# Kernel optimization log

Hardware: AMD Instinct MI355X
Metric: run time of the kernel (lower is better)

The kernel has to match this reference:

```python
import jax, jax.numpy as jnp
import numpy as np

LN_EPS = 1e-5
N_HEADS = 8

def _layernorm(x, g, b):
    mu = jnp.mean(x, axis=-1, keepdims=True)
    var = jnp.var(x, axis=-1, keepdims=True)
    return (x - mu) * jax.lax.rsqrt(var + LN_EPS) * g + b

def _posenc(seqlen, d_model, dtype):
    den = jnp.exp(-jnp.arange(0, d_model, 2, dtype=dtype) * (np.log(10000.0) / d_model))
    pos = jnp.arange(seqlen, dtype=dtype)[:, None]  # [S,1]
    pe = jnp.zeros((seqlen, d_model), dtype=dtype)
    pe = pe.at[:, 0::2].set(jnp.sin(pos * den))
    pe = pe.at[:, 1::2].set(jnp.cos(pos * den)[:, : d_model // 2])
    return pe  # [S,d]

def setup_inputs() -> dict:
    key = jax.random.key(0)
    ks = jax.random.split(key, 12)
    B, S, V, D, F, L, DL = 64, 256, 16, 512, 2048, 6, 256
    s = 0.05
    return {
        "src_pad": jax.random.normal(ks[0], (B, S, V), jnp.float32),
        "emb_w": jax.random.normal(ks[1], (D, V), jnp.float32) * s,
        "emb_b": jnp.zeros((D,), jnp.float32),
        "qkv_w": jax.random.normal(ks[2], (L, 3 * D, D), jnp.float32) * s,
        "qkv_b": jnp.zeros((L, 3 * D), jnp.float32),
        "out_w": jax.random.normal(ks[3], (L, D, D), jnp.float32) * s,
        "out_b": jnp.zeros((L, D), jnp.float32),
        "ff1_w": jax.random.normal(ks[4], (L, F, D), jnp.float32) * s,
        "ff1_b": jnp.zeros((L, F), jnp.float32),
        "ff2_w": jax.random.normal(ks[5], (L, D, F), jnp.float32) * s,
        "ff2_b": jnp.zeros((L, D), jnp.float32),
        "ln1_g": jnp.ones((L, D), jnp.float32),
        "ln1_b": jnp.zeros((L, D), jnp.float32),
        "ln2_g": jnp.ones((L, D), jnp.float32),
        "ln2_b": jnp.zeros((L, D), jnp.float32),
        "lat_w": jax.random.normal(ks[6], (DL, S * D), jnp.float32) * 0.005,
        "lat_b": jnp.zeros((DL,), jnp.float32),
        "head_w": jax.random.normal(ks[7], (1, DL), jnp.float32) * s,
        "head_b": jnp.zeros((1,), jnp.float32),
    }

def reference(src_pad, emb_w, emb_b, qkv_w, qkv_b, out_w, out_b,
              ff1_w, ff1_b, ff2_w, ff2_b, ln1_g, ln1_b, ln2_g, ln2_b,
              lat_w, lat_b, head_w, head_b):
    B, S, V = src_pad.shape
    D = emb_w.shape[0]
    L = qkv_w.shape[0]
    H = N_HEADS
    dh = D // H
    # batched replacement of the per-token Python-loop embedding
    x = jnp.einsum('bsv,dv->bsd', src_pad, emb_w) + emb_b
    x = x + _posenc(S, D, x.dtype)  # dropout is identity at eval
    scale = 1.0 / np.sqrt(dh)
    for l in range(L):  # post-norm PyTorch TransformerEncoderLayer, relu FFN
        qkv = jnp.einsum('bsd,ed->bse', x, qkv_w[l]) + qkv_b[l]  # [B,S,3D]
        q, k, v = jnp.split(qkv, 3, axis=-1)
        q = q.reshape(B, S, H, dh).transpose(0, 2, 1, 3)
        k = k.reshape(B, S, H, dh).transpose(0, 2, 1, 3)
        v = v.reshape(B, S, H, dh).transpose(0, 2, 1, 3)
        attn = jax.nn.softmax(jnp.einsum('bhqd,bhkd->bhqk', q, k) * scale, axis=-1)
        o = jnp.einsum('bhqk,bhkd->bhqd', attn, v).transpose(0, 2, 1, 3).reshape(B, S, D)
        o = jnp.einsum('bsd,ed->bse', o, out_w[l]) + out_b[l]
        x = _layernorm(x + o, ln1_g[l], ln1_b[l])
        h = jax.nn.relu(jnp.einsum('bsd,fd->bsf', x, ff1_w[l]) + ff1_b[l])
        h = jnp.einsum('bsf,df->bsd', h, ff2_w[l]) + ff2_b[l]
        x = _layernorm(x + h, ln2_g[l], ln2_b[l])
    mem = x.reshape(B, S * D) @ lat_w.T + lat_b  # [B, d_latent]
    pred = jax.nn.sigmoid(mem @ head_w.T + head_b)  # [B,1]
    return pred
```

## Files before the change

### kernel.cpp

```cpp
#include <hip/hip_runtime.h>
#include <hip/hip_bf16.h>
#include <cstdint>

#define DEV static __device__ __forceinline__

typedef __attribute__((ext_vector_type(8))) short bf16x8;
typedef __attribute__((ext_vector_type(4))) float f32x4;

DEV unsigned short f2bf(float f) {
  union { float f; unsigned u; } c; c.f = f;
  unsigned u = c.u;
  return (unsigned short)((u + 0x7fffu + ((u >> 16) & 1u)) >> 16);
}
DEV float bf2f(unsigned short h) {
  union { unsigned u; float f; } c; c.u = ((unsigned)h) << 16; return c.f;
}
DEV float bflo(unsigned u) { union { unsigned u; float f; } c; c.u = u << 16; return c.f; }
DEV float bfhi(unsigned u) { union { unsigned u; float f; } c; c.u = u & 0xffff0000u; return c.f; }
DEV unsigned pack_bf16(float a, float b) {
  union { float f; unsigned u; } ca, cb; ca.f = a; cb.f = b;
  return __builtin_amdgcn_perm(cb.u + 0x8000u, ca.u + 0x8000u, 0x07060302u);
}

#define ASYNC_COPY16(gsrc, ldst)                                                      \
  __builtin_amdgcn_global_load_lds(                                                   \
      (const __attribute__((address_space(1))) void*)(unsigned long long)(gsrc),      \
      (__attribute__((address_space(3))) void*)(unsigned int)(unsigned long long)(ldst), \
      16, 0, 0)

__global__ void cvt4_kernel(const float* __restrict__ s, unsigned short* __restrict__ d) {
  size_t i = ((size_t)blockIdx.x * 256 + threadIdx.x) * 4;
  float4 v = *(const float4*)(s + i);
  d[i + 0] = f2bf(v.x);
  d[i + 1] = f2bf(v.y);
  d[i + 2] = f2bf(v.z);
  d[i + 3] = f2bf(v.w);
}

__global__ void embed_kernel(const float* __restrict__ src,
                             const float* __restrict__ emb_w,
                             const float* __restrict__ emb_b,
                             unsigned short* __restrict__ xb) {
  const int bs = blockIdx.x;
  const int d = threadIdx.x;
  const int s = bs & 255;
  __shared__ float sv[16];
  if (d < 16) sv[d] = src[(size_t)bs * 16 + d];
  __syncthreads();
  const float* wr = emb_w + (size_t)d * 16;
  float acc = emb_b[d];
#pragma unroll
  for (int v = 0; v < 16; v++) acc += sv[v] * wr[v];
  const float den = __expf(-(float)(d & ~1) * (9.2103403719761836f / 512.f));
  const float arg = (float)s * den;
  acc += (d & 1) ? __cosf(arg) : __sinf(arg);
  xb[(size_t)bs * 512 + d] = f2bf(acc);
}

template <int BN, int MINW, int RELU, int OUT_BF16, int ADD_RES>
__global__ __launch_bounds__(256, MINW) void gemm_nt(
    const unsigned short* __restrict__ A,
    const unsigned short* __restrict__ B,
    const float* __restrict__ bias,
    const unsigned short* __restrict__ res,
    float* __restrict__ Cf,
    unsigned short* __restrict__ Cb,
    int M, int N, int K) {
  constexpr int MT = (BN == 128) ? 4 : 2;
  constexpr int NT = 4;
  __shared__ unsigned short As[128 * 64];
  __shared__ unsigned short Bs[BN * 64];
  const int tid = threadIdx.x;
  const int lane = tid & 63;
  const int w = tid >> 6;
  const int m0 = blockIdx.x * 128;
  const int n0 = blockIdx.y * BN;

  const int srow = lane >> 3;
  const int scol = (((lane & 7) ^ srow)) * 8;
  const unsigned short* gA0 = A + (size_t)(m0 + w * 32 + srow) * K + scol;
  unsigned short* lA0 = As + (w * 32) * 64;
  constexpr int BROWS = BN / 4 / 8;
  const unsigned short* gB0 = B + (size_t)(n0 + w * (BN / 4) + srow) * K + scol;
  unsigned short* lB0 = Bs + (w * (BN / 4)) * 64;

  const int wm = (BN == 128) ? (w >> 1) * 64 : w * 32;
  const int wn = (BN == 128) ? (w & 1) * 64 : 0;
  const int r16 = lane & 15;
  const int quad = lane >> 4;
  const int rsw = r16 & 7;

  f32x4 acc[MT][NT] = {};

  for (int k0 = 0; k0 < K; k0 += 64) {
#pragma unroll
    for (int i = 0; i < 4; i++)
      ASYNC_COPY16(gA0 + (size_t)(i * 8) * K + k0, lA0 + i * 512);
#pragma unroll
    for (int i = 0; i < BROWS; i++)
      ASYNC_COPY16(gB0 + (size_t)(i * 8) * K + k0, lB0 + i * 512);
    __syncthreads();
#pragma unroll
    for (int kh = 0; kh < 2; kh++) {
      const int ko = ((kh * 4 + quad) ^ rsw) * 8;
      bf16x8 xa[MT], wb[NT];
#pragma unroll
      for (int i = 0; i < MT; i++)
        xa[i] = *(const bf16x8*)(As + (wm + i * 16 + r16) * 64 + ko);
#pragma unroll
      for (int j = 0; j < NT; j++)
        wb[j] = *(const bf16x8*)(Bs + (wn + j * 16 + r16) * 64 + ko);
#pragma unroll
      for (int i = 0; i < MT; i++)
#pragma unroll
        for (int j = 0; j < NT; j++)
          acc[i][j] = __builtin_amdgcn_mfma_f32_16x16x32_bf16(wb[j], xa[i], acc[i][j], 0, 0, 0);
    }
    __syncthreads();
  }

  const int mb = m0 + wm + r16;
  const int nb = n0 + wn + quad * 4;
#pragma unroll
  for (int j = 0; j < NT; j++) {
    const int n = nb + j * 16;
    const float4 bv = *(const float4*)(bias + n);
#pragma unroll
    for (int i = 0; i < MT; i++) {
      const size_t off = (size_t)(mb + i * 16) * N + n;
      float4 v;
      v.x = acc[i][j][0] + bv.x;
      v.y = acc[i][j][1] + bv.y;
      v.z = acc[i][j][2] + bv.z;
      v.w = acc[i][j][3] + bv.w;
      if (ADD_RES) {
        const uint2 ru = *(const uint2*)(res + off);
        v.x += bflo(ru.x); v.y += bfhi(ru.x);
        v.z += bflo(ru.y); v.w += bfhi(ru.y);
      }
      if (RELU) {
        v.x = fmaxf(v.x, 0.f); v.y = fmaxf(v.y, 0.f);
        v.z = fmaxf(v.z, 0.f); v.w = fmaxf(v.w, 0.f);
      }
      if (OUT_BF16) {
        uint2 u;
        u.x = pack_bf16(v.x, v.y);
        u.y = pack_bf16(v.z, v.w);
        *(uint2*)(Cb + off) = u;
      } else {
        *(float4*)(Cf + off) = v;
      }
    }
  }
}

__global__ __launch_bounds__(256, 2) void attn_fused(
    const unsigned short* __restrict__ qkv,
    unsigned short* __restrict__ O) {
  __shared__ unsigned short Vt[64 * 264];
  __shared__ unsigned short Pl[32 * 264];
  __shared__ float redM[4][32];
  __shared__ float redS[4][32];
  const int tid = threadIdx.x;
  const int lane = tid & 63;
  const int w = tid >> 6;
  const int r16 = lane & 15;
  const int quad = lane >> 4;
  const int h = blockIdx.x & 7;
  const int b = blockIdx.x >> 3;

  {
    const int kp = w * 32 + (lane & 31);
    const int dhalf = lane >> 5;
    const unsigned short* vbase =
        qkv + (size_t)(b * 256 + 2 * kp) * 1536 + 1024 + h * 64;
    unsigned* dst = (unsigned*)Vt;
#pragma unroll
    for (int t = 0; t < 4; t++) {
      const int dc = dhalf + 2 * t;
      const uint4 a = *(const uint4*)(vbase + dc * 8);
      const uint4 bb = *(const uint4*)(vbase + 1536 + dc * 8);
      const unsigned* ap = (const unsigned*)&a;
      const unsigned* bp = (const unsigned*)&bb;
#pragma unroll
      for (int i = 0; i < 4; i++) {
        const unsigned lo = ap[i], hi = bp[i];
        dst[(dc * 8 + 2 * i) * 132 + kp] = (lo & 0xffffu) | (hi << 16);
        dst[(dc * 8 + 2 * i + 1) * 132 + kp] = (lo >> 16) | (hi & 0xffff0000u);
      }
    }
  }
  __syncthreads();

  const unsigned short* krow =
      qkv + (size_t)(b * 256 + r16) * 1536 + 512 + h * 64 + quad * 8;
  const unsigned short* qrow =
      qkv + (size_t)(b * 256 + r16) * 1536 + h * 64 + quad * 8;

  for (int qt = 0; qt < 8; qt++) {
    const int q0 = qt * 32;
    f32x4 acc[4][2] = {};
    bf16x8 bQ0[2], bQ1[2];
#pragma unroll
    for (int nt = 0; nt < 2; nt++) {
      const unsigned short* qp = qrow + (size_t)(q0 + nt * 16) * 1536;
      bQ0[nt] = *(const bf16x8*)(qp);
      bQ1[nt] = *(const bf16x8*)(qp + 32);
    }
#pragma unroll
    for (int mt = 0; mt < 4; mt++) {
      const unsigned short* kp = krow + (size_t)(w * 64 + mt * 16) * 1536;
      const bf16x8 aK0 = *(const bf16x8*)(kp);
      const bf16x8 aK1 = *(const bf16x8*)(kp + 32);
#pragma unroll
      for (int nt = 0; nt < 2; nt++) {
        acc[mt][nt] = __builtin_amdgcn_mfma_f32_16x16x32_bf16(aK0, bQ0[nt], acc[mt][nt], 0, 0, 0);
        acc[mt][nt] = __builtin_amdgcn_mfma_f32_16x16x32_bf16(aK1, bQ1[nt], acc[mt][nt], 0, 0, 0);
      }
    }
#pragma unroll
    for (int nt = 0; nt < 2; nt++) {
      float m = acc[0][nt][0];
#pragma unroll
      for (int mt = 0; mt < 4; mt++)
#pragma unroll
        for (int r = 0; r < 4; r++) m = fmaxf(m, acc[mt][nt][r]);
      m = fmaxf(m, __shfl_xor(m, 16));
      m = fmaxf(m, __shfl_xor(m, 32));
      if (quad == 0) redM[w][nt * 16 + r16] = m;
    }
    __syncthreads();
    float mg[2], sw[2];
#pragma unroll
    for (int nt = 0; nt < 2; nt++) {
      const int q = nt * 16 + r16;
      mg[nt] = fmaxf(fmaxf(redM[0][q], redM[1][q]), fmaxf(redM[2][q], redM[3][q]));
      sw[nt] = 0.f;
    }
#pragma unroll
    for (int mt = 0; mt < 4; mt++)
#pragma unroll
      for (int nt = 0; nt < 2; nt++)
#pragma unroll
        for (int r = 0; r < 4; r++) {
          acc[mt][nt][r] = __expf((acc[mt][nt][r] - mg[nt]) * 0.125f);
          sw[nt] += acc[mt][nt][r];
        }
#pragma unroll
    for (int nt = 0; nt < 2; nt++) {
      sw[nt] += __shfl_xor(sw[nt], 16);
      sw[nt] += __shfl_xor(sw[nt], 32);
      if (quad == 0) redS[w][nt * 16 + r16] = sw[nt];
    }
    __syncthreads();
    float inv[2];
#pragma unroll
    for (int nt = 0; nt < 2; nt++) {
      const int q = nt * 16 + r16;
      inv[nt] = 1.f / (redS[0][q] + redS[1][q] + redS[2][q] + redS[3][q]);
    }
#pragma unroll
    for (int nt = 0; nt < 2; nt++) {
      unsigned short* prow = Pl + (nt * 16 + r16) * 264 + w * 64 + quad * 4;
#pragma unroll
      for (int mt = 0; mt < 4; mt++) {
        uint2 u;
        u.x = pack_bf16(acc[mt][nt][0] * inv[nt], acc[mt][nt][1] * inv[nt]);
        u.y = pack_bf16(acc[mt][nt][2] * inv[nt], acc[mt][nt][3] * inv[nt]);
        *(uint2*)(prow + mt * 16) = u;
      }
    }
    __syncthreads();
    f32x4 o[2] = {};
#pragma unroll
    for (int s = 0; s < 8; s++) {
      const bf16x8 aV = *(const bf16x8*)(Vt + (w * 16 + r16) * 264 + s * 32 + quad * 8);
#pragma unroll
      for (int nt = 0; nt < 2; nt++) {
        const bf16x8 bP = *(const bf16x8*)(Pl + (nt * 16 + r16) * 264 + s * 32 + quad * 8);
        o[nt] = __builtin_amdgcn_mfma_f32_16x16x32_bf16(aV, bP, o[nt], 0, 0, 0);
      }
    }
#pragma unroll
    for (int nt = 0; nt < 2; nt++) {
      uint2 u;
      u.x = pack_bf16(o[nt][0], o[nt][1]);
      u.y = pack_bf16(o[nt][2], o[nt][3]);
      *(uint2*)(O + (size_t)(b * 256 + q0 + nt * 16 + r16) * 512 + h * 64 +
                w * 16 + quad * 4) = u;
    }
  }
}

__global__ __launch_bounds__(256) void ln_kernel(
    const float* __restrict__ z, const float* __restrict__ g,
    const float* __restrict__ bb, unsigned short* __restrict__ xb) {
  const int row = blockIdx.x;
  const int tid = threadIdx.x;
  const size_t base = (size_t)row * 512;
  float v0 = z[base + tid];
  float v1 = z[base + tid + 256];
  float s = v0 + v1, ss = v0 * v0 + v1 * v1;
#pragma unroll
  for (int off = 32; off > 0; off >>= 1) {
    s += __shfl_xor(s, off);
    ss += __shfl_xor(ss, off);
  }
  __shared__ float red[8];
  const int w = tid >> 6, lane = tid & 63;
  if (lane == 0) { red[w * 2] = s; red[w * 2 + 1] = ss; }
  __syncthreads();
  s = red[0] + red[2] + red[4] + red[6];
  ss = red[1] + red[3] + red[5] + red[7];
  const float mu = s * (1.f / 512.f);
  const float var = ss * (1.f / 512.f) - mu * mu;
  const float rs = rsqrtf(var + 1e-5f);
  const float o0 = (v0 - mu) * rs * g[tid] + bb[tid];
  const float o1 = (v1 - mu) * rs * g[tid + 256] + bb[tid + 256];
  xb[base + tid] = f2bf(o0);
  xb[base + tid + 256] = f2bf(o1);
}

__global__ void zero_kernel(float* __restrict__ p) {
  p[blockIdx.x * 256 + threadIdx.x] = 0.f;
}

__global__ __launch_bounds__(256) void latent_gemm(
    const unsigned short* __restrict__ xb, const float* __restrict__ W,
    float* __restrict__ mem) {
  const int tid = threadIdx.x;
  const int lane = tid & 63;
  const int w = tid >> 6;
  const int r16 = lane & 15;
  const int quad = lane >> 4;
  const int n0 = blockIdx.x * 64 + w * 16;
  const int kc0 = blockIdx.y * 1024;

  const float* wrow = W + (size_t)(n0 + r16) * 131072 + kc0 + quad * 8;
  const unsigned short* xrow = xb + (size_t)r16 * 131072 + kc0 + quad * 8;

  f32x4 c[4] = {};
  for (int k = 0; k < 1024; k += 32) {
    const float4 wa = *(const float4*)(wrow + k);
    const float4 wb = *(const float4*)(wrow + k + 4);
    union { unsigned u[4]; bf16x8 v; } cw;
    cw.u[0] = pack_bf16(wa.x, wa.y);
    cw.u[1] = pack_bf16(wa.z, wa.w);
    cw.u[2] = pack_bf16(wb.x, wb.y);
    cw.u[3] = pack_bf16(wb.z, wb.w);
#pragma unroll
    for (int i = 0; i < 4; i++) {
      const bf16x8 aX = *(const bf16x8*)(xrow + (size_t)i * 2097152 + k);
      c[i] = __builtin_amdgcn_mfma_f32_16x16x32_bf16(aX, cw.v, c[i], 0, 0, 0);
    }
  }
#pragma unroll
  for (int i = 0; i < 4; i++)
#pragma unroll
    for (int r = 0; r < 4; r++)
      atomicAdd(&mem[(size_t)(i * 16 + quad * 4 + r) * 256 + n0 + r16], c[i][r]);
}

__global__ __launch_bounds__(256) void head_kernel(
    const float* __restrict__ mem, const float* __restrict__ lat_b,
    const float* __restrict__ head_w, const float* __restrict__ head_b,
    float* __restrict__ out) {
  const int b = blockIdx.x;
  const int tid = threadIdx.x;
  float v = (mem[(size_t)b * 256 + tid] + lat_b[tid]) * head_w[tid];
#pragma unroll
  for (int off = 32; off > 0; off >>= 1) v += __shfl_xor(v, off);
  __shared__ float red[4];
  const int w = tid >> 6, lane = tid & 63;
  if (lane == 0) red[w] = v;
  __syncthreads();
  if (tid == 0) {
    const float z = red[0] + red[1] + red[2] + red[3] + head_b[0];
    out[b] = 1.f / (1.f + __expf(-z));
  }
}

extern "C" void kernel_launch(void* const* d_in, const int* in_sizes, int n_in,
                              void* d_out, int out_size, void* d_ws, size_t ws_size,
                              hipStream_t stream) {
  (void)in_sizes; (void)n_in; (void)out_size; (void)ws_size;
  const float* src_pad = (const float*)d_in[0];
  const float* emb_w = (const float*)d_in[1];
  const float* emb_b = (const float*)d_in[2];
  const float* qkv_w = (const float*)d_in[3];
  const float* qkv_b = (const float*)d_in[4];
  const float* out_w = (const float*)d_in[5];
  const float* out_b = (const float*)d_in[6];
  const float* ff1_w = (const float*)d_in[7];
  const float* ff1_b = (const float*)d_in[8];
  const float* ff2_w = (const float*)d_in[9];
  const float* ff2_b = (const float*)d_in[10];
  const float* ln1_g = (const float*)d_in[11];
  const float* ln1_b = (const float*)d_in[12];
  const float* ln2_g = (const float*)d_in[13];
  const float* ln2_b = (const float*)d_in[14];
  const float* lat_w = (const float*)d_in[15];
  const float* lat_b = (const float*)d_in[16];
  const float* head_w = (const float*)d_in[17];
  const float* head_b = (const float*)d_in[18];
  float* out = (float*)d_out;

  char* p = (char*)d_ws;
  unsigned short* xb = (unsigned short*)p; p += (size_t)16384 * 512 * 2;
  unsigned short* qkv = (unsigned short*)p;
  float* y = (float*)qkv;
  p += (size_t)16384 * 1536 * 2;
  unsigned short* attno = (unsigned short*)p; p += (size_t)16384 * 512 * 2;
  unsigned short* h = (unsigned short*)p;     p += (size_t)16384 * 2048 * 2;
  unsigned short* wq = (unsigned short*)p;    p += (size_t)4718592 * 2;
  unsigned short* wo = (unsigned short*)p;    p += (size_t)1572864 * 2;
  unsigned short* wf1 = (unsigned short*)p;   p += (size_t)6291456 * 2;
  unsigned short* wf2 = (unsigned short*)p;   p += (size_t)6291456 * 2;
  float* mem = (float*)p;           p += (size_t)16384 * 4;

  cvt4_kernel<<<4608, 256, 0, stream>>>(qkv_w, wq);
  cvt4_kernel<<<1536, 256, 0, stream>>>(out_w, wo);
  cvt4_kernel<<<6144, 256, 0, stream>>>(ff1_w, wf1);
  cvt4_kernel<<<6144, 256, 0, stream>>>(ff2_w, wf2);

  embed_kernel<<<16384, 512, 0, stream>>>(src_pad, emb_w, emb_b, xb);

  for (int l = 0; l < 6; l++) {
    gemm_nt<128, 3, 0, 1, 0><<<dim3(128, 12), 256, 0, stream>>>(
        xb, wq + (size_t)l * 786432, qkv_b + (size_t)l * 1536, nullptr,
        nullptr, qkv, 16384, 1536, 512);
    attn_fused<<<512, 256, 0, stream>>>(qkv, attno);
    gemm_nt<64, 4, 0, 0, 1><<<dim3(128, 8), 256, 0, stream>>>(
        attno, wo + (size_t)l * 262144, out_b + (size_t)l * 512, xb,
        y, nullptr, 16384, 512, 512);
    ln_kernel<<<16384, 256, 0, stream>>>(y, ln1_g + (size_t)l * 512,
                                         ln1_b + (size_t)l * 512, xb);
    gemm_nt<128, 3, 1, 1, 0><<<dim3(128, 16), 256, 0, stream>>>(
        xb, wf1 + (size_t)l * 1048576, ff1_b + (size_t)l * 2048, nullptr,
        nullptr, h, 16384, 2048, 512);
    gemm_nt<64, 4, 0, 0, 1><<<dim3(128, 8), 256, 0, stream>>>(
        h, wf2 + (size_t)l * 1048576, ff2_b + (size_t)l * 512, xb,
        y, nullptr, 16384, 512, 2048);
    ln_kernel<<<16384, 256, 0, stream>>>(y, ln2_g + (size_t)l * 512,
                                         ln2_b + (size_t)l * 512, xb);
  }

  zero_kernel<<<64, 256, 0, stream>>>(mem);
  latent_gemm<<<dim3(4, 128), 256, 0, stream>>>(xb, lat_w, mem);
  head_kernel<<<64, 256, 0, stream>>>(mem, lat_b, head_w, head_b, out);
}
```

Measured before the change: 1.611 ms.

## Replace GEMM with double-buffered 512-thread pipelined kernel using larger tiles

Replaces the single-buffered gemm_nt with gemm_pipe. It uses 8 waves, BN=256 and BM of 128 or 256, and double-buffers LDS so the next K-tile's async global-to-LDS copies are issued in phases between MFMA groups. It also raises wave priority during MFMA issue. The aim is to hide global load latency and raise data reuse per block. In exchange it uses more LDS (up to 128KB per block), fewer blocks for the N=512 GEMMs (256 blocks), and adds extra barriers per K step.

```diff
diff --git a/kernel.cpp b/kernel.cpp
--- a/kernel.cpp
+++ b/kernel.cpp
@@ -57,8 +57,8 @@
   xb[(size_t)bs * 512 + d] = f2bf(acc);
 }
 
-template <int BN, int MINW, int RELU, int OUT_BF16, int ADD_RES>
-__global__ __launch_bounds__(256, MINW) void gemm_nt(
+template <int BM, int RELU, int OUT_BF16, int ADD_RES>
+__global__ __launch_bounds__(512, 2) void gemm_pipe(
     const unsigned short* __restrict__ A,
     const unsigned short* __restrict__ B,
     const float* __restrict__ bias,
@@ -66,67 +66,98 @@
     float* __restrict__ Cf,
     unsigned short* __restrict__ Cb,
     int M, int N, int K) {
-  constexpr int MT = (BN == 128) ? 4 : 2;
+  constexpr int BN = 256;
+  constexpr int MT = BM / 32;
   constexpr int NT = 4;
-  __shared__ unsigned short As[128 * 64];
-  __shared__ unsigned short Bs[BN * 64];
+  constexpr int NLA = BM / 64;
+  constexpr int NL = NLA + 4;
+  __shared__ unsigned short lds[2][(BM + BN) * 64];
+
   const int tid = threadIdx.x;
   const int lane = tid & 63;
   const int w = tid >> 6;
-  const int m0 = blockIdx.x * 128;
-  const int n0 = blockIdx.y * BN;
-
-  const int srow = lane >> 3;
-  const int scol = (((lane & 7) ^ srow)) * 8;
-  const unsigned short* gA0 = A + (size_t)(m0 + w * 32 + srow) * K + scol;
-  unsigned short* lA0 = As + (w * 32) * 64;
-  constexpr int BROWS = BN / 4 / 8;
-  const unsigned short* gB0 = B + (size_t)(n0 + w * (BN / 4) + srow) * K + scol;
-  unsigned short* lB0 = Bs + (w * (BN / 4)) * 64;
-
-  const int wm = (BN == 128) ? (w >> 1) * 64 : w * 32;
-  const int wn = (BN == 128) ? (w & 1) * 64 : 0;
+  const int wmi = w >> 2;
+  const int wni = w & 3;
   const int r16 = lane & 15;
   const int quad = lane >> 4;
   const int rsw = r16 & 7;
+  const int m0 = blockIdx.x * BM;
+  const int n0 = blockIdx.y * BN;
+
+  const int srow = tid >> 3;
+  const int scol = ((tid & 7) ^ (srow & 7)) * 8;
+  const unsigned short* gA = A + (size_t)(m0 + srow) * K + scol;
+  const unsigned short* gB = B + (size_t)(n0 + srow) * K + scol;
+
+#define STG(i, bufi, kc)                                                        \
+  do {                                                                          \
+    if ((i) < NLA)                                                              \
+      ASYNC_COPY16(gA + (size_t)((i) * 64) * K + (kc),                          \
+                   &lds[(bufi)][((i) * 64 + w * 8) * 64]);                      \
+    else                                                                        \
+      ASYNC_COPY16(gB + (size_t)(((i) - NLA) * 64) * K + (kc),                  \
+                   &lds[(bufi)][(BM + ((i) - NLA) * 64 + w * 8) * 64]);         \
+  } while (0)
 
   f32x4 acc[MT][NT] = {};
 
-  for (int k0 = 0; k0 < K; k0 += 64) {
-#pragma unroll
-    for (int i = 0; i < 4; i++)
-      ASYNC_COPY16(gA0 + (size_t)(i * 8) * K + k0, lA0 + i * 512);
-#pragma unroll
-    for (int i = 0; i < BROWS; i++)
-      ASYNC_COPY16(gB0 + (size_t)(i * 8) * K + k0, lB0 + i * 512);
-    __syncthreads();
-#pragma unroll
-    for (int kh = 0; kh < 2; kh++) {
-      const int ko = ((kh * 4 + quad) ^ rsw) * 8;
-      bf16x8 xa[MT], wb[NT];
-#pragma unroll
-      for (int i = 0; i < MT; i++)
-        xa[i] = *(const bf16x8*)(As + (wm + i * 16 + r16) * 64 + ko);
-#pragma unroll
-      for (int j = 0; j < NT; j++)
-        wb[j] = *(const bf16x8*)(Bs + (wn + j * 16 + r16) * 64 + ko);
-#pragma unroll
-      for (int i = 0; i < MT; i++)
-#pragma unroll
-        for (int j = 0; j < NT; j++)
-          acc[i][j] = __builtin_amdgcn_mfma_f32_16x16x32_bf16(wb[j], xa[i], acc[i][j], 0, 0, 0);
-    }
-    __syncthreads();
-  }
-
-  const int mb = m0 + wm + r16;
-  const int nb = n0 + wn + quad * 4;
-#pragma unroll
-  for (int j = 0; j < NT; j++) {
+#pragma unroll
+  for (int i = 0; i < NL; ++i) STG(i, 0, 0);
+
+  const int NK = K >> 6;
+  for (int kt = 0; kt < NK; ++kt) {
+    const int buf = kt & 1;
+    asm volatile("s_waitcnt vmcnt(0)" ::: "memory");
+    __builtin_amdgcn_s_barrier();
+    const unsigned short* As = &lds[buf][0];
+    const unsigned short* Bs = &lds[buf][BM * 64];
+    const int doStage = (kt + 1 < NK);
+    const int kc = (kt + 1) << 6;
+    const int sb = buf ^ 1;
+    bf16x8 aR[MT];
+#pragma unroll
+    for (int kh = 0; kh < 2; ++kh) {
+#pragma unroll
+      for (int nh = 0; nh < 2; ++nh) {
+        const int ph = kh * 2 + nh;
+        const int ko = ((kh * 4 + quad) ^ rsw) * 8;
+        if (nh == 0) {
+#pragma unroll
+          for (int m = 0; m < MT; ++m)
+            aR[m] = *(const bf16x8*)(As + (wmi * (MT * 16) + m * 16 + r16) * 64 + ko);
+        }
+        bf16x8 bR[2];
+#pragma unroll
+        for (int j = 0; j < 2; ++j)
+          bR[j] = *(const bf16x8*)(Bs + (wni * 64 + (nh * 2 + j) * 16 + r16) * 64 + ko);
+        if (doStage) {
+          if (2 * ph < NL) STG(2 * ph, sb, kc);
+          if (2 * ph + 1 < NL) STG(2 * ph + 1, sb, kc);
+        }
+        __builtin_amdgcn_s_barrier();
+        asm volatile("s_waitcnt lgkmcnt(0)" ::: "memory");
+        __builtin_amdgcn_s_setprio(1);
+#pragma unroll
+        for (int m = 0; m < MT; ++m)
+#pragma unroll
+          for (int j = 0; j < 2; ++j)
+            acc[m][nh * 2 + j] = __builtin_amdgcn_mfma_f32_16x16x32_bf16(
+                bR[j], aR[m], acc[m][nh * 2 + j], 0, 0, 0);
+        __builtin_amdgcn_s_setprio(0);
+        __builtin_amdgcn_s_barrier();
+      }
+    }
+  }
+#undef STG
+
+  const int mb = m0 + wmi * (MT * 16) + r16;
+  const int nb = n0 + wni * 64 + quad * 4;
+#pragma unroll
+  for (int j = 0; j < NT; ++j) {
     const int n = nb + j * 16;
     const float4 bv = *(const float4*)(bias + n);
 #pragma unroll
-    for (int i = 0; i < MT; i++) {
+    for (int i = 0; i < MT; ++i) {
       const size_t off = (size_t)(mb + i * 16) * N + n;
       float4 v;
       v.x = acc[i][j][0] + bv.x;
@@ -426,19 +457,19 @@
   embed_kernel<<<16384, 512, 0, stream>>>(src_pad, emb_w, emb_b, xb);
 
   for (int l = 0; l < 6; l++) {
-    gemm_nt<128, 3, 0, 1, 0><<<dim3(128, 12), 256, 0, stream>>>(
+    gemm_pipe<128, 0, 1, 0><<<dim3(128, 6), 512, 0, stream>>>(
         xb, wq + (size_t)l * 786432, qkv_b + (size_t)l * 1536, nullptr,
         nullptr, qkv, 16384, 1536, 512);
     attn_fused<<<512, 256, 0, stream>>>(qkv, attno);
-    gemm_nt<64, 4, 0, 0, 1><<<dim3(128, 8), 256, 0, stream>>>(
+    gemm_pipe<128, 0, 0, 1><<<dim3(128, 2), 512, 0, stream>>>(
         attno, wo + (size_t)l * 262144, out_b + (size_t)l * 512, xb,
         y, nullptr, 16384, 512, 512);
     ln_kernel<<<16384, 256, 0, stream>>>(y, ln1_g + (size_t)l * 512,
                                          ln1_b + (size_t)l * 512, xb);
-    gemm_nt<128, 3, 1, 1, 0><<<dim3(128, 16), 256, 0, stream>>>(
+    gemm_pipe<256, 1, 1, 0><<<dim3(64, 8), 512, 0, stream>>>(
         xb, wf1 + (size_t)l * 1048576, ff1_b + (size_t)l * 2048, nullptr,
         nullptr, h, 16384, 2048, 512);
-    gemm_nt<64, 4, 0, 0, 1><<<dim3(128, 8), 256, 0, stream>>>(
+    gemm_pipe<128, 0, 0, 1><<<dim3(128, 2), 512, 0, stream>>>(
         h, wf2 + (size_t)l * 1048576, ff2_b + (size_t)l * 512, xb,
         y, nullptr, 16384, 512, 2048);
     ln_kernel<<<16384, 256, 0, stream>>>(y, ln2_g + (size_t)l * 512,
```

Result: slower. 1.652 ms (+2.6%).
